# Optimization experiments

Hardware: AMD Instinct MI355X
Metric: run time of the kernel (lower is better)

The kernel has to match this reference:

```python
import jax, jax.numpy as jnp
import numpy as np

B, HW, E, H, L, T = 256, 196, 1024, 1024, 128, 48
FC_OUT = L + H + 2  # label | topic | temp | stop


def _linear_params(k, out_d, in_d):
    k1, k2 = jax.random.split(k)
    bound = 1.0 / np.sqrt(in_d)
    W = jax.random.uniform(k1, (out_d, in_d), jnp.float32, -bound, bound)
    b = jax.random.uniform(k2, (out_d,), jnp.float32, -bound, bound)
    return W, b


def setup_inputs() -> dict:
    key = jax.random.key(0)
    ks = jax.random.split(key, 8)
    image = jax.random.normal(ks[0], (B, HW, E), jnp.float32)
    label = jax.random.uniform(ks[1], (B, T, L), jnp.float32)
    # lengths sorted descending (the torch module uses @length_sorted)
    length = jnp.sort(jax.random.randint(ks[2], (B,), 1, T + 1))[::-1]
    W_h, b_h = _linear_params(ks[3], H, E)
    W_m, b_m = _linear_params(ks[4], H, E)
    W_ih, b_ih = _linear_params(ks[5], 4 * H, E + L)
    W_hh, b_hh = _linear_params(ks[6], 4 * H, H)
    W_fc, b_fc = _linear_params(ks[7], FC_OUT, H)
    return {"image": image, "label": label, "length": length,
            "W_h": W_h, "b_h": b_h, "W_m": W_m, "b_m": b_m,
            "W_ih": W_ih, "W_hh": W_hh, "b_ih": b_ih, "b_hh": b_hh,
            "W_fc": W_fc, "b_fc": b_fc}


def reference(image, label, length, W_h, b_h, W_m, b_m, W_ih, W_hh, b_ih, b_hh, W_fc, b_fc):
    # dropout is identity (eval mode)
    img_mean = image.mean(axis=1)                       # (B, E)
    h0 = jnp.tanh(img_mean @ W_h.T + b_h)               # (B, H)
    m0 = jnp.tanh(img_mean @ W_m.T + b_m)               # (B, H)
    lab_t_major = jnp.transpose(label, (1, 0, 2))       # (T, B, L)
    ts = jnp.arange(T)

    def step(carry, inp):
        h, m = carry
        lab_t, t = inp
        x = jnp.concatenate([img_mean, lab_t], axis=-1)          # (B, E+L)
        gates = x @ W_ih.T + b_ih + h @ W_hh.T + b_hh            # (B, 4H), torch order i,f,g,o
        i, f, g, o = jnp.split(gates, 4, axis=-1)
        m = jax.nn.sigmoid(f) * m + jax.nn.sigmoid(i) * jnp.tanh(g)
        h = jax.nn.sigmoid(o) * jnp.tanh(m)
        out = jax.nn.relu(h @ W_fc.T + b_fc)                     # (B, L+H+2)
        _label = out[:, :L]
        _topic = out[:, L:L + H]
        _temp = jnp.exp(out[:, L + H:L + H + 1])
        _stop = jax.nn.sigmoid(out[:, L + H + 1:])
        mask = (t < length)[:, None].astype(out.dtype)           # pad_sequence zero-padding
        return (h, m), (_label * mask, _topic * mask, _temp * mask, _stop * mask)

    _, (lab_o, top_o, temp_o, stop_o) = jax.lax.scan(step, (h0, m0), (lab_t_major, ts))
    # scan stacks on time axis -> (T, B, D); return batch-major (B, T, D)
    return tuple(jnp.transpose(a, (1, 0, 2)) for a in (lab_o, top_o, temp_o, stop_o))
```

## Files before the change

kernel.cpp:

```cpp
#include <hip/hip_runtime.h>

typedef float f32x4 __attribute__((ext_vector_type(4)));
typedef short s16x8 __attribute__((ext_vector_type(8)));
typedef unsigned short u16;

#define B_    256
#define HW_   196
#define E_    1024
#define H_    1024
#define L_    128
#define T_    48
#define FCOUT 1154
#define FCPAD 1216

#define GJOBS 128
#define FJOBS 76
#define NBLK  (GJOBS + FJOBS)

__device__ __forceinline__ u16 f2bf(float x) {
  union { float f; unsigned u; } v; v.f = x;
  unsigned r = v.u + 0x7FFF + ((v.u >> 16) & 1);
  return (u16)(r >> 16);
}
__device__ __forceinline__ float sigm(float x) { return 1.f / (1.f + expf(-x)); }

__device__ __forceinline__ uint2 ld_h8(const u16* p) {
  unsigned long long v = __hip_atomic_load((const unsigned long long*)p,
                                           __ATOMIC_RELAXED, __HIP_MEMORY_SCOPE_AGENT);
  union { unsigned long long u; uint2 d; } c; c.u = v; return c.d;
}
__device__ __forceinline__ void st_h8(u16* p, ushort4 s) {
  union { ushort4 s; unsigned long long u; } c; c.s = s;
  __hip_atomic_store((unsigned long long*)p, c.u,
                     __ATOMIC_RELAXED, __HIP_MEMORY_SCOPE_AGENT);
}

__device__ __forceinline__ void gbar(int* cnt, int it) {
  __syncthreads();
  if (threadIdx.x == 0) {
    __hip_atomic_fetch_add(cnt, 1, __ATOMIC_RELAXED, __HIP_MEMORY_SCOPE_AGENT);
    const int target = NBLK * (it + 1);
    while (__hip_atomic_load(cnt, __ATOMIC_RELAXED, __HIP_MEMORY_SCOPE_AGENT) < target)
      __builtin_amdgcn_s_sleep(2);
  }
  __syncthreads();
}

__global__ __launch_bounds__(256) void cvt_bf16_v4(
    const float* __restrict__ in, u16* __restrict__ out,
    int src_rows, int in_ld, int in_off, int cols4, long total4) {
  long idx = (long)blockIdx.x * 256 + threadIdx.x;
  if (idx >= total4) return;
  int r  = (int)(idx / cols4);
  int c4 = (int)(idx % cols4) * 4;
  f32x4 v = {0.f, 0.f, 0.f, 0.f};
  if (r < src_rows) v = *(const f32x4*)&in[(size_t)r * in_ld + in_off + c4];
  ushort4 o;
  ((u16*)&o)[0] = f2bf(v[0]); ((u16*)&o)[1] = f2bf(v[1]);
  ((u16*)&o)[2] = f2bf(v[2]); ((u16*)&o)[3] = f2bf(v[3]);
  *(ushort4*)&out[idx * 4] = o;
}

__global__ __launch_bounds__(256) void img_mean_k(
    const float* __restrict__ image, u16* __restrict__ meanB) {
  int idx = blockIdx.x * 256 + threadIdx.x;
  int b  = idx >> 8;
  int e4 = (idx & 255) * 4;
  const float* p = image + (size_t)b * HW_ * E_ + e4;
  f32x4 s = {0.f, 0.f, 0.f, 0.f};
  #pragma unroll 4
  for (int hw = 0; hw < HW_; ++hw) s += *(const f32x4*)&p[(size_t)hw * E_];
  ushort4 o;
  #pragma unroll
  for (int c = 0; c < 4; ++c) ((u16*)&o)[c] = f2bf(s[c] * (1.0f / HW_));
  *(ushort4*)&meanB[(size_t)b * E_ + e4] = o;
}

template <int MODE>
__global__ __launch_bounds__(256) void gemm_nt(
    const u16* __restrict__ A, int lda, const u16* __restrict__ Bp, int ldb, int K,
    const float* __restrict__ bias1, const float* __restrict__ bias2,
    float* __restrict__ outF, u16* __restrict__ outB, int ldc) {
  __shared__ __align__(16) u16 As[64][72];
  __shared__ __align__(16) u16 Bs[64][72];

  const int m0 = blockIdx.x * 64;
  const int n0 = blockIdx.y * 64;
  const int tid  = threadIdx.x;
  const int lane = tid & 63;
  const int wave = tid >> 6;
  const int wm = wave & 1, wn = wave >> 1;
  const int quad = lane >> 4, l16 = lane & 15;
  const int loadRow = tid >> 3;
  const int loadCol = (tid & 7) * 8;

  f32x4 acc[2][2] = {};

  for (int kb = 0; kb < K; kb += 64) {
    __syncthreads();
    #pragma unroll
    for (int p = 0; p < 2; ++p) {
      int r = loadRow + p * 32;
      *(uint4*)&As[r][loadCol] = *(const uint4*)&A [(size_t)(m0 + r) * lda + kb + loadCol];
      *(uint4*)&Bs[r][loadCol] = *(const uint4*)&Bp[(size_t)(n0 + r) * ldb + kb + loadCol];
    }
    __syncthreads();
    #pragma unroll
    for (int ks = 0; ks < 64; ks += 32) {
      s16x8 a0v = *(const s16x8*)&As[wm * 32      + l16][ks + quad * 8];
      s16x8 a1v = *(const s16x8*)&As[wm * 32 + 16 + l16][ks + quad * 8];
      s16x8 b0v = *(const s16x8*)&Bs[wn * 32      + l16][ks + quad * 8];
      s16x8 b1v = *(const s16x8*)&Bs[wn * 32 + 16 + l16][ks + quad * 8];
      acc[0][0] = __builtin_amdgcn_mfma_f32_16x16x32_bf16(a0v, b0v, acc[0][0], 0, 0, 0);
      acc[0][1] = __builtin_amdgcn_mfma_f32_16x16x32_bf16(a0v, b1v, acc[0][1], 0, 0, 0);
      acc[1][0] = __builtin_amdgcn_mfma_f32_16x16x32_bf16(a1v, b0v, acc[1][0], 0, 0, 0);
      acc[1][1] = __builtin_amdgcn_mfma_f32_16x16x32_bf16(a1v, b1v, acc[1][1], 0, 0, 0);
    }
  }

  #pragma unroll
  for (int mi = 0; mi < 2; ++mi) {
    #pragma unroll
    for (int ni = 0; ni < 2; ++ni) {
      #pragma unroll
      for (int r = 0; r < 4; ++r) {
        int m = m0 + wm * 32 + mi * 16 + quad * 4 + r;
        int n = n0 + wn * 32 + ni * 16 + l16;
        float v = acc[mi][ni][r];
        if constexpr (MODE == 0) {
          outF[(size_t)m * ldc + n] = v + bias1[n] + bias2[n];
        } else if constexpr (MODE == 1) {
          outB[(size_t)m * ldc + n] = f2bf(tanhf(v + bias1[n]));
        } else {
          outF[(size_t)m * ldc + n] = tanhf(v + bias1[n]);
        }
      }
    }
  }
}

struct GS8 { u16 A[2][32][72]; u16 B[2][256][72]; };
struct FS8 { u16 A[2][64][72]; u16 B[2][64][72]; };
union __align__(16) SharedU {
  GS8 g;
  FS8 f;
  float gs[2][4][32][68];
  float fs[64][68];
};

__global__ __launch_bounds__(512) void scan_k(
    const u16* __restrict__ labB,
    const u16* __restrict__ WihL,
    const u16* __restrict__ WhhB,
    const u16* __restrict__ WfcB,
    const float* __restrict__ gbase,
    const float* __restrict__ b_fc,
    u16* __restrict__ hb0, u16* __restrict__ hb1,
    const float* __restrict__ mS0,
    const int* __restrict__ length,
    float* __restrict__ out,
    int* __restrict__ barCnt) {
  __shared__ SharedU sh;
  __shared__ __align__(16) float gbs[4][32][64];

  const int bid  = blockIdx.x;
  const int tid  = threadIdx.x;
  const int g2   = tid >> 8;
  const int gtid = tid & 255;
  const int lane = tid & 63;
  const int wave = tid >> 6;
  const int sw   = wave & 3;
  const int quad = lane >> 4, l16 = lane & 15;
  const int ar = gtid >> 3;
  const int ac = (gtid & 7) * 8;

  const bool isG = bid < GJOBS;
  int mb = 0, jb = 0, m0 = 0, n0 = 0, glen = 0;
  f32x4 mreg = {0.f, 0.f, 0.f, 0.f};

  if (isG) {
    jb = (bid & 7) * 2 + ((bid >> 3) & 1);
    mb = bid >> 4;
    glen = length[mb * 32];
    const int bl = tid >> 4, j4 = (tid & 15) * 4;
    #pragma unroll
    for (int g = 0; g < 4; ++g)
      *(f32x4*)&gbs[g][bl][j4] =
          *(const f32x4*)&gbase[(size_t)(mb * 32 + bl) * (4 * H_) + g * H_ + jb * 64 + j4];
    mreg = *(const f32x4*)&mS0[(size_t)(mb * 32 + bl) * H_ + jb * 64 + j4];
  } else {
    const int fid = bid - GJOBS;
    m0 = (fid / 19) * 64;
    n0 = (fid % 19) * 64;
    glen = length[m0];
  }

  for (int p = 0; p <= T_; ++p) {
    u16* hcur  = (p & 1) ? hb1 : hb0;
    u16* hnext = (p & 1) ? hb0 : hb1;

    if (isG) {
      if (p < T_ && glen > p) {
        f32x4 acc[2][4] = {};
        for (int kb = 0; kb < 9; ++kb) {
          const int seg1 = (g2 == 1) || (kb >= 2);
          const int k0 = g2 ? (448 + kb * 64) : (seg1 ? (kb - 2) * 64 : kb * 64);
          __syncthreads();
          if (seg1) {
            const u16* Ap = hcur + (size_t)(mb * 32 + ar) * H_ + k0 + ac;
            *(uint2*)&sh.g.A[g2][ar][ac]     = ld_h8(Ap);
            *(uint2*)&sh.g.A[g2][ar][ac + 4] = ld_h8(Ap + 4);
          } else {
            *(uint4*)&sh.g.A[g2][ar][ac] = *(const uint4*)
                &labB[(size_t)(mb * 32 + ar) * (T_ * L_) + (size_t)p * L_ + k0 + ac];
          }
          const u16* Bw  = seg1 ? WhhB : WihL;
          const int  ldb = seg1 ? H_ : L_;
          #pragma unroll
          for (int q = 0; q < 8; ++q) {
            int rr = ar + q * 32;
            int grow = (rr >> 6) * H_ + jb * 64 + (rr & 63);
            *(uint4*)&sh.g.B[g2][rr][ac] =
                *(const uint4*)&Bw[(size_t)grow * ldb + k0 + ac];
          }
          __syncthreads();
          #pragma unroll
          for (int ks = 0; ks < 64; ks += 32) {
            s16x8 av[2], bv[4];
            av[0] = *(const s16x8*)&sh.g.A[g2][l16][ks + quad * 8];
            av[1] = *(const s16x8*)&sh.g.A[g2][16 + l16][ks + quad * 8];
            #pragma unroll
            for (int ni = 0; ni < 4; ++ni)
              bv[ni] = *(const s16x8*)&sh.g.B[g2][sw * 64 + ni * 16 + l16][ks + quad * 8];
            #pragma unroll
            for (int mi = 0; mi < 2; ++mi)
              #pragma unroll
              for (int ni = 0; ni < 4; ++ni)
                acc[mi][ni] = __builtin_amdgcn_mfma_f32_16x16x32_bf16(
                    av[mi], bv[ni], acc[mi][ni], 0, 0, 0);
          }
        }

        __syncthreads();
        #pragma unroll
        for (int mi = 0; mi < 2; ++mi)
          #pragma unroll
          for (int ni = 0; ni < 4; ++ni)
            #pragma unroll
            for (int r = 0; r < 4; ++r)
              sh.gs[g2][sw][mi * 16 + quad * 4 + r][ni * 16 + l16] = acc[mi][ni][r];
        __syncthreads();

        {
          const int bl = tid >> 4, j4 = (tid & 15) * 4;
          f32x4 gi = *(const f32x4*)&sh.gs[0][0][bl][j4] + *(const f32x4*)&sh.gs[1][0][bl][j4];
          f32x4 gf = *(const f32x4*)&sh.gs[0][1][bl][j4] + *(const f32x4*)&sh.gs[1][1][bl][j4];
          f32x4 gg = *(const f32x4*)&sh.gs[0][2][bl][j4] + *(const f32x4*)&sh.gs[1][2][bl][j4];
          f32x4 go = *(const f32x4*)&sh.gs[0][3][bl][j4] + *(const f32x4*)&sh.gs[1][3][bl][j4];
          f32x4 bi  = *(const f32x4*)&gbs[0][bl][j4];
          f32x4 bff = *(const f32x4*)&gbs[1][bl][j4];
          f32x4 bg  = *(const f32x4*)&gbs[2][bl][j4];
          f32x4 bo  = *(const f32x4*)&gbs[3][bl][j4];
          ushort4 hb;
          #pragma unroll
          for (int c = 0; c < 4; ++c) {
            float I = sigm(gi[c] + bi[c]);
            float F = sigm(gf[c] + bff[c]);
            float G = tanhf(gg[c] + bg[c]);
            float O = sigm(go[c] + bo[c]);
            float mm = F * mreg[c] + I * G;
            mreg[c] = mm;
            ((u16*)&hb)[c] = f2bf(O * tanhf(mm));
          }
          st_h8(&hnext[(size_t)(mb * 32 + bl) * H_ + jb * 64 + j4], hb);
        }
      }
    } else if (p >= 1) {
      const int t = p - 1;
      if (glen > t) {
        const int wm = sw & 1, wn = sw >> 1;
        f32x4 acc[2][2] = {};
        for (int kb = 0; kb < 8; ++kb) {
          const int k0 = g2 * 512 + kb * 64;
          __syncthreads();
          #pragma unroll
          for (int pp = 0; pp < 2; ++pp) {
            int r = ar + pp * 32;
            const u16* Ap = hcur + (size_t)(m0 + r) * H_ + k0 + ac;
            *(uint2*)&sh.f.A[g2][r][ac]     = ld_h8(Ap);
            *(uint2*)&sh.f.A[g2][r][ac + 4] = ld_h8(Ap + 4);
            *(uint4*)&sh.f.B[g2][r][ac] =
                *(const uint4*)&WfcB[(size_t)(n0 + r) * H_ + k0 + ac];
          }
          __syncthreads();
          #pragma unroll
          for (int ks = 0; ks < 64; ks += 32) {
            s16x8 a0v = *(const s16x8*)&sh.f.A[g2][wm * 32      + l16][ks + quad * 8];
            s16x8 a1v = *(const s16x8*)&sh.f.A[g2][wm * 32 + 16 + l16][ks + quad * 8];
            s16x8 b0v = *(const s16x8*)&sh.f.B[g2][wn * 32      + l16][ks + quad * 8];
            s16x8 b1v = *(const s16x8*)&sh.f.B[g2][wn * 32 + 16 + l16][ks + quad * 8];
            acc[0][0] = __builtin_amdgcn_mfma_f32_16x16x32_bf16(a0v, b0v, acc[0][0], 0, 0, 0);
            acc[0][1] = __builtin_amdgcn_mfma_f32_16x16x32_bf16(a0v, b1v, acc[0][1], 0, 0, 0);
            acc[1][0] = __builtin_amdgcn_mfma_f32_16x16x32_bf16(a1v, b0v, acc[1][0], 0, 0, 0);
            acc[1][1] = __builtin_amdgcn_mfma_f32_16x16x32_bf16(a1v, b1v, acc[1][1], 0, 0, 0);
          }
        }

        __syncthreads();
        if (g2 == 1) {
          #pragma unroll
          for (int mi = 0; mi < 2; ++mi)
            #pragma unroll
            for (int ni = 0; ni < 2; ++ni)
              #pragma unroll
              for (int r = 0; r < 4; ++r)
                sh.fs[wm * 32 + mi * 16 + quad * 4 + r][wn * 32 + ni * 16 + l16] =
                    acc[mi][ni][r];
        }
        __syncthreads();
        if (g2 == 0) {
          #pragma unroll
          for (int mi = 0; mi < 2; ++mi) {
            #pragma unroll
            for (int ni = 0; ni < 2; ++ni) {
              #pragma unroll
              for (int r = 0; r < 4; ++r) {
                int ml = wm * 32 + mi * 16 + quad * 4 + r;
                int nl = wn * 32 + ni * 16 + l16;
                int m = m0 + ml;
                int n = n0 + nl;
                if (n < FCOUT) {
                  float rv = fmaxf(acc[mi][ni][r] + sh.fs[ml][nl] + b_fc[n], 0.f);
                  float msk = (t < length[m]) ? 1.f : 0.f;
                  if (n < L_) {
                    out[(size_t)m * (T_ * L_) + t * L_ + n] = rv * msk;
                  } else if (n < L_ + H_) {
                    out[(size_t)(B_ * T_ * L_) + (size_t)m * (T_ * H_) + t * H_ + (n - L_)] = rv * msk;
                  } else if (n == L_ + H_) {
                    out[(size_t)B_ * T_ * (L_ + H_) + m * T_ + t] = expf(rv) * msk;
                  } else {
                    out[(size_t)B_ * T_ * (L_ + H_ + 1) + m * T_ + t] = sigm(rv) * msk;
                  }
                }
              }
            }
          }
        }
      } else if (n0 == 0) {
        f32x4 z = {0.f, 0.f, 0.f, 0.f};
        for (int i = tid; i < 64 * 32; i += 512) {
          int r = i >> 5, c4 = (i & 31) * 4;
          *(f32x4*)&out[(size_t)(m0 + r) * (T_ * L_) + t * L_ + c4] = z;
        }
        for (int i = tid; i < 64 * 256; i += 512) {
          int r = i >> 8, c4 = (i & 255) * 4;
          *(f32x4*)&out[(size_t)(B_ * T_ * L_) + (size_t)(m0 + r) * (T_ * H_) + t * H_ + c4] = z;
        }
        if (tid < 64) {
          out[(size_t)B_ * T_ * (L_ + H_) + (m0 + tid) * T_ + t] = 0.f;
          out[(size_t)B_ * T_ * (L_ + H_ + 1) + (m0 + tid) * T_ + t] = 0.f;
        }
      }
    }

    gbar(barCnt, p);
  }
}

extern "C" void kernel_launch(void* const* d_in, const int* in_sizes, int n_in,
                              void* d_out, int out_size, void* d_ws, size_t ws_size,
                              hipStream_t stream) {
  const float* image  = (const float*)d_in[0];
  const float* label  = (const float*)d_in[1];
  const int*   length = (const int*)  d_in[2];
  const float* W_h    = (const float*)d_in[3];
  const float* b_h    = (const float*)d_in[4];
  const float* W_m    = (const float*)d_in[5];
  const float* b_m    = (const float*)d_in[6];
  const float* W_ih   = (const float*)d_in[7];
  const float* W_hh   = (const float*)d_in[8];
  const float* b_ih   = (const float*)d_in[9];
  const float* b_hh   = (const float*)d_in[10];
  const float* W_fc   = (const float*)d_in[11];
  const float* b_fc   = (const float*)d_in[12];
  float* out = (float*)d_out;

  char* ws = (char*)d_ws;
  size_t off = 0;
  auto alloc = [&](size_t bytes) -> void* {
    void* p = ws + off;
    off = (off + bytes + 255) & ~(size_t)255;
    return p;
  };
  u16*   meanB = (u16*)  alloc((size_t)B_ * E_ * 2);
  u16*   WhB   = (u16*)  alloc((size_t)H_ * E_ * 2);
  u16*   WmB   = (u16*)  alloc((size_t)H_ * E_ * 2);
  u16*   WihE  = (u16*)  alloc((size_t)4 * H_ * E_ * 2);
  u16*   WihL  = (u16*)  alloc((size_t)4 * H_ * L_ * 2);
  u16*   WhhB  = (u16*)  alloc((size_t)4 * H_ * H_ * 2);
  u16*   WfcB  = (u16*)  alloc((size_t)FCPAD * H_ * 2);
  u16*   labB  = (u16*)  alloc((size_t)B_ * T_ * L_ * 2);
  float* gbase = (float*)alloc((size_t)B_ * 4 * H_ * 4);
  u16*   hbuf0 = (u16*)  alloc((size_t)B_ * H_ * 2);
  u16*   hbuf1 = (u16*)  alloc((size_t)B_ * H_ * 2);
  float* mS    = (float*)alloc((size_t)B_ * H_ * 4);
  int*   bar   = (int*)  alloc(256);

  auto cvt = [&](const float* in, u16* o, int rows, int src_rows, int in_ld,
                 int in_off, int cols) {
    long total4 = (long)rows * cols / 4;
    int blocks = (int)((total4 + 255) / 256);
    cvt_bf16_v4<<<blocks, 256, 0, stream>>>(in, o, src_rows, in_ld, in_off,
                                            cols / 4, total4);
  };

  cvt(W_h,  WhB,  H_,     H_,     E_,      0,  E_);
  cvt(W_m,  WmB,  H_,     H_,     E_,      0,  E_);
  cvt(W_ih, WihE, 4 * H_, 4 * H_, E_ + L_, 0,  E_);
  cvt(W_ih, WihL, 4 * H_, 4 * H_, E_ + L_, E_, L_);
  cvt(W_hh, WhhB, 4 * H_, 4 * H_, H_,      0,  H_);
  cvt(W_fc, WfcB, FCPAD,  FCOUT,  H_,      0,  H_);
  cvt(label, labB, B_, B_, T_ * L_, 0, T_ * L_);

  img_mean_k<<<(B_ * E_ / 4) / 256, 256, 0, stream>>>(image, meanB);

  gemm_nt<1><<<dim3(B_ / 64, H_ / 64), 256, 0, stream>>>(
      meanB, E_, WhB, E_, E_, b_h, nullptr, nullptr, hbuf0, H_);
  gemm_nt<2><<<dim3(B_ / 64, H_ / 64), 256, 0, stream>>>(
      meanB, E_, WmB, E_, E_, b_m, nullptr, mS, nullptr, H_);
  gemm_nt<0><<<dim3(B_ / 64, (4 * H_) / 64), 256, 0, stream>>>(
      meanB, E_, WihE, E_, E_, b_ih, b_hh, gbase, nullptr, 4 * H_);

  hipMemsetAsync(bar, 0, 8, stream);
  scan_k<<<NBLK, 512, 0, stream>>>(
      labB, WihL, WhhB, WfcB, gbase, b_fc, hbuf0, hbuf1, mS, length, out, bar);
}
```

Measured before the change: 1.403 ms.

## Split grid barrier into producer/consumer counters with triple-buffered hidden state

Replaces the all-blocks grid barrier with a packed 64-bit counter: gate blocks bump the low half and FC blocks bump the high half. Each role waits only on the producers it actually depends on, which lets gate blocks run ahead of the FC blocks by one step. The hidden state becomes a three-slot ring buffer so that run-ahead is safe. Weight and label tiles are now prefetched before the wait, and all h tiles are loaded into registers up front, to hide latency. This adds register pressure, and the relaxed-atomic ordering is subtle.

```diff
diff --git a/kernel.cpp b/kernel.cpp
--- a/kernel.cpp
+++ b/kernel.cpp
@@ -35,15 +35,21 @@
                      __ATOMIC_RELAXED, __HIP_MEMORY_SCOPE_AGENT);
 }
 
-__device__ __forceinline__ void gbar(int* cnt, int it) {
-  __syncthreads();
+__device__ __forceinline__ void bar_wait(unsigned long long* bar,
+                                         unsigned lot, unsigned hit) {
   if (threadIdx.x == 0) {
-    __hip_atomic_fetch_add(cnt, 1, __ATOMIC_RELAXED, __HIP_MEMORY_SCOPE_AGENT);
-    const int target = NBLK * (it + 1);
-    while (__hip_atomic_load(cnt, __ATOMIC_RELAXED, __HIP_MEMORY_SCOPE_AGENT) < target)
+    for (;;) {
+      unsigned long long v = __hip_atomic_load(bar, __ATOMIC_RELAXED,
+                                               __HIP_MEMORY_SCOPE_AGENT);
+      if ((unsigned)v >= lot && (unsigned)(v >> 32) >= hit) break;
       __builtin_amdgcn_s_sleep(2);
+    }
   }
   __syncthreads();
+}
+__device__ __forceinline__ void bar_add(unsigned long long* bar,
+                                        unsigned long long v) {
+  __hip_atomic_fetch_add(bar, v, __ATOMIC_RELAXED, __HIP_MEMORY_SCOPE_AGENT);
 }
 
 __global__ __launch_bounds__(256) void cvt_bf16_v4(
@@ -155,11 +161,11 @@
     const u16* __restrict__ WfcB,
     const float* __restrict__ gbase,
     const float* __restrict__ b_fc,
-    u16* __restrict__ hb0, u16* __restrict__ hb1,
+    u16* __restrict__ hs0, u16* __restrict__ hs1, u16* __restrict__ hs2,
     const float* __restrict__ mS0,
     const int* __restrict__ length,
     float* __restrict__ out,
-    int* __restrict__ barCnt) {
+    unsigned long long* __restrict__ bar) {
   __shared__ SharedU sh;
   __shared__ __align__(16) float gbs[4][32][64];
 
@@ -173,6 +179,8 @@
   const int quad = lane >> 4, l16 = lane & 15;
   const int ar = gtid >> 3;
   const int ac = (gtid & 7) * 8;
+
+  u16* slot[3] = {hs0, hs1, hs2};
 
   const bool isG = bid < GJOBS;
   int mb = 0, jb = 0, m0 = 0, n0 = 0, glen = 0;
@@ -194,34 +202,87 @@
     n0 = (fid % 19) * 64;
     glen = length[m0];
   }
+  __syncthreads();
 
   for (int p = 0; p <= T_; ++p) {
-    u16* hcur  = (p & 1) ? hb1 : hb0;
-    u16* hnext = (p & 1) ? hb0 : hb1;
+    u16* hc = slot[p % 3];
+    u16* hn = slot[(p + 1) % 3];
 
     if (isG) {
-      if (p < T_ && glen > p) {
-        f32x4 acc[2][4] = {};
-        for (int kb = 0; kb < 9; ++kb) {
-          const int seg1 = (g2 == 1) || (kb >= 2);
-          const int k0 = g2 ? (448 + kb * 64) : (seg1 ? (kb - 2) * 64 : kb * 64);
-          __syncthreads();
-          if (seg1) {
-            const u16* Ap = hcur + (size_t)(mb * 32 + ar) * H_ + k0 + ac;
-            *(uint2*)&sh.g.A[g2][ar][ac]     = ld_h8(Ap);
-            *(uint2*)&sh.g.A[g2][ar][ac + 4] = ld_h8(Ap + 4);
-          } else {
-            *(uint4*)&sh.g.A[g2][ar][ac] = *(const uint4*)
-                &labB[(size_t)(mb * 32 + ar) * (T_ * L_) + (size_t)p * L_ + k0 + ac];
-          }
-          const u16* Bw  = seg1 ? WhhB : WihL;
-          const int  ldb = seg1 ? H_ : L_;
+      if (p == T_) break;
+      const bool live = glen > p;
+
+      uint4 lA1;
+      if (live) {
+        {
+          const u16* Bw  = g2 ? WhhB : WihL;
+          const int  ldb = g2 ? H_ : L_;
+          const int  k0b = g2 ? 448 : 0;
           #pragma unroll
           for (int q = 0; q < 8; ++q) {
             int rr = ar + q * 32;
             int grow = (rr >> 6) * H_ + jb * 64 + (rr & 63);
             *(uint4*)&sh.g.B[g2][rr][ac] =
-                *(const uint4*)&Bw[(size_t)grow * ldb + k0 + ac];
+                *(const uint4*)&Bw[(size_t)grow * ldb + k0b + ac];
+          }
+          if (g2 == 0) {
+            const u16* Lp = labB + (size_t)(mb * 32 + ar) * (T_ * L_) +
+                            (size_t)p * L_ + ac;
+            *(uint4*)&sh.g.A[0][ar][ac] = *(const uint4*)Lp;
+            lA1 = *(const uint4*)(Lp + 64);
+          }
+        }
+      }
+      bar_wait(bar, 128u * (unsigned)p,
+               (p >= 2) ? 76u * (unsigned)(p - 1) : 0u);
+
+      if (live) {
+        uint2 hA[9][2];
+        const u16* hrow = hc + (size_t)(mb * 32 + ar) * H_ + ac;
+        if (g2 == 0) {
+          #pragma unroll
+          for (int s = 0; s < 7; ++s) {
+            hA[s][0] = ld_h8(hrow + s * 64);
+            hA[s][1] = ld_h8(hrow + s * 64 + 4);
+          }
+        } else {
+          #pragma unroll
+          for (int s = 0; s < 9; ++s) {
+            hA[s][0] = ld_h8(hrow + 448 + s * 64);
+            hA[s][1] = ld_h8(hrow + 448 + s * 64 + 4);
+          }
+        }
+
+        f32x4 acc[2][4] = {};
+        #pragma unroll
+        for (int kb = 0; kb < 9; ++kb) {
+          if (kb == 0) {
+            if (g2 == 1) {
+              *(uint2*)&sh.g.A[1][ar][ac]     = hA[0][0];
+              *(uint2*)&sh.g.A[1][ar][ac + 4] = hA[0][1];
+            }
+          } else {
+            __syncthreads();
+            if (kb == 1 && g2 == 0) {
+              *(uint4*)&sh.g.A[0][ar][ac] = lA1;
+            } else if (g2 == 0) {
+              *(uint2*)&sh.g.A[0][ar][ac]     = hA[kb - 2][0];
+              *(uint2*)&sh.g.A[0][ar][ac + 4] = hA[kb - 2][1];
+            } else {
+              *(uint2*)&sh.g.A[1][ar][ac]     = hA[kb][0];
+              *(uint2*)&sh.g.A[1][ar][ac + 4] = hA[kb][1];
+            }
+            const int seg1 = (g2 == 1) || (kb >= 2);
+            const int k0 = g2 ? (448 + kb * 64) : (seg1 ? (kb - 2) * 64 : kb * 64);
+            const u16* Bw  = seg1 ? WhhB : WihL;
+            const int  ldb = seg1 ? H_ : L_;
+            #pragma unroll
+            for (int q = 0; q < 8; ++q) {
+              int rr = ar + q * 32;
+              int grow = (rr >> 6) * H_ + jb * 64 + (rr & 63);
+              *(uint4*)&sh.g.B[g2][rr][ac] =
+                  *(const uint4*)&Bw[(size_t)grow * ldb + k0 + ac];
+            }
           }
           __syncthreads();
           #pragma unroll
@@ -272,25 +333,51 @@
             mreg[c] = mm;
             ((u16*)&hb)[c] = f2bf(O * tanhf(mm));
           }
-          st_h8(&hnext[(size_t)(mb * 32 + bl) * H_ + jb * 64 + j4], hb);
-        }
+          st_h8(&hn[(size_t)(mb * 32 + bl) * H_ + jb * 64 + j4], hb);
+        }
+        __syncthreads();
       }
-    } else if (p >= 1) {
+      if (tid == 0) bar_add(bar, 1ull);
+    } else {
       const int t = p - 1;
-      if (glen > t) {
+      const bool liveF = (p >= 1) && (glen > t);
+
+      if (liveF) {
+        #pragma unroll
+        for (int pp = 0; pp < 2; ++pp) {
+          int r = ar + pp * 32;
+          *(uint4*)&sh.f.B[g2][r][ac] =
+              *(const uint4*)&WfcB[(size_t)(n0 + r) * H_ + g2 * 512 + ac];
+        }
+      }
+      bar_wait(bar, 128u * (unsigned)((p <= T_) ? p : T_), 0u);
+
+      if (liveF) {
+        uint2 fA[8][2][2];
+        #pragma unroll
+        for (int kb = 0; kb < 8; ++kb) {
+          #pragma unroll
+          for (int pp = 0; pp < 2; ++pp) {
+            const u16* Ap = hc + (size_t)(m0 + ar + pp * 32) * H_ +
+                            g2 * 512 + kb * 64 + ac;
+            fA[kb][pp][0] = ld_h8(Ap);
+            fA[kb][pp][1] = ld_h8(Ap + 4);
+          }
+        }
+
         const int wm = sw & 1, wn = sw >> 1;
         f32x4 acc[2][2] = {};
+        #pragma unroll
         for (int kb = 0; kb < 8; ++kb) {
-          const int k0 = g2 * 512 + kb * 64;
-          __syncthreads();
+          if (kb > 0) __syncthreads();
           #pragma unroll
           for (int pp = 0; pp < 2; ++pp) {
             int r = ar + pp * 32;
-            const u16* Ap = hcur + (size_t)(m0 + r) * H_ + k0 + ac;
-            *(uint2*)&sh.f.A[g2][r][ac]     = ld_h8(Ap);
-            *(uint2*)&sh.f.A[g2][r][ac + 4] = ld_h8(Ap + 4);
-            *(uint4*)&sh.f.B[g2][r][ac] =
-                *(const uint4*)&WfcB[(size_t)(n0 + r) * H_ + k0 + ac];
+            *(uint2*)&sh.f.A[g2][r][ac]     = fA[kb][pp][0];
+            *(uint2*)&sh.f.A[g2][r][ac + 4] = fA[kb][pp][1];
+            if (kb > 0)
+              *(uint4*)&sh.f.B[g2][r][ac] =
+                  *(const uint4*)&WfcB[(size_t)(n0 + r) * H_ + g2 * 512 + kb * 64 + ac];
           }
           __syncthreads();
           #pragma unroll
@@ -307,6 +394,7 @@
         }
 
         __syncthreads();
+        if (tid == 0) bar_add(bar, 1ull << 32);
         if (g2 == 1) {
           #pragma unroll
           for (int mi = 0; mi < 2; ++mi)
@@ -346,24 +434,25 @@
             }
           }
         }
-      } else if (n0 == 0) {
-        f32x4 z = {0.f, 0.f, 0.f, 0.f};
-        for (int i = tid; i < 64 * 32; i += 512) {
-          int r = i >> 5, c4 = (i & 31) * 4;
-          *(f32x4*)&out[(size_t)(m0 + r) * (T_ * L_) + t * L_ + c4] = z;
-        }
-        for (int i = tid; i < 64 * 256; i += 512) {
-          int r = i >> 8, c4 = (i & 255) * 4;
-          *(f32x4*)&out[(size_t)(B_ * T_ * L_) + (size_t)(m0 + r) * (T_ * H_) + t * H_ + c4] = z;
-        }
-        if (tid < 64) {
-          out[(size_t)B_ * T_ * (L_ + H_) + (m0 + tid) * T_ + t] = 0.f;
-          out[(size_t)B_ * T_ * (L_ + H_ + 1) + (m0 + tid) * T_ + t] = 0.f;
-        }
+      } else {
+        if (p >= 1 && n0 == 0) {
+          f32x4 z = {0.f, 0.f, 0.f, 0.f};
+          for (int i = tid; i < 64 * 32; i += 512) {
+            int r = i >> 5, c4 = (i & 31) * 4;
+            *(f32x4*)&out[(size_t)(m0 + r) * (T_ * L_) + t * L_ + c4] = z;
+          }
+          for (int i = tid; i < 64 * 256; i += 512) {
+            int r = i >> 8, c4 = (i & 255) * 4;
+            *(f32x4*)&out[(size_t)(B_ * T_ * L_) + (size_t)(m0 + r) * (T_ * H_) + t * H_ + c4] = z;
+          }
+          if (tid < 64) {
+            out[(size_t)B_ * T_ * (L_ + H_) + (m0 + tid) * T_ + t] = 0.f;
+            out[(size_t)B_ * T_ * (L_ + H_ + 1) + (m0 + tid) * T_ + t] = 0.f;
+          }
+        }
+        if (tid == 0) bar_add(bar, 1ull << 32);
       }
     }
-
-    gbar(barCnt, p);
   }
 }
 
@@ -403,8 +492,9 @@
   float* gbase = (float*)alloc((size_t)B_ * 4 * H_ * 4);
   u16*   hbuf0 = (u16*)  alloc((size_t)B_ * H_ * 2);
   u16*   hbuf1 = (u16*)  alloc((size_t)B_ * H_ * 2);
+  u16*   hbuf2 = (u16*)  alloc((size_t)B_ * H_ * 2);
   float* mS    = (float*)alloc((size_t)B_ * H_ * 4);
-  int*   bar   = (int*)  alloc(256);
+  unsigned long long* bar = (unsigned long long*)alloc(256);
 
   auto cvt = [&](const float* in, u16* o, int rows, int src_rows, int in_ld,
                  int in_off, int cols) {
@@ -433,5 +523,6 @@
 
   hipMemsetAsync(bar, 0, 8, stream);
   scan_k<<<NBLK, 512, 0, stream>>>(
-      labB, WihL, WhhB, WfcB, gbase, b_fc, hbuf0, hbuf1, mS, length, out, bar);
-}
+      labB, WihL, WhhB, WfcB, gbase, b_fc, hbuf0, hbuf1, hbuf2, mS, length,
+      out, bar);
+}
```

After: 1.492 ms. 6.3% more time.

## Stage full h rows in LDS once per step; read weights directly from global

Applied to the files above, without the earlier changes.

The recurrent scan kernel no longer stages A and B tiles through double-buffered shared memory with two barriers per k-block. Each step now copies the whole hidden-state slab for the block into padded LDS behind a single barrier. MFMA operands for W_hh, W_ih, W_fc and the label input are loaded straight from global memory (expected to hit L2 or cache) into registers. The gate bias is also read from global each step instead of being kept in LDS. This removes many per-step syncs and LDS writes, at the cost of uncoalesced global weight loads and higher register pressure from fully unrolled loops.

```diff
diff --git a/kernel.cpp b/kernel.cpp
--- a/kernel.cpp
+++ b/kernel.cpp
@@ -16,6 +16,8 @@
 #define GJOBS 128
 #define FJOBS 76
 #define NBLK  (GJOBS + FJOBS)
+
+#define HPAD  1032
 
 __device__ __forceinline__ u16 f2bf(float x) {
   union { float f; unsigned u; } v; v.f = x;
@@ -139,11 +141,8 @@
   }
 }
 
-struct GS8 { u16 A[2][32][72]; u16 B[2][256][72]; };
-struct FS8 { u16 A[2][64][72]; u16 B[2][64][72]; };
 union __align__(16) SharedU {
-  GS8 g;
-  FS8 f;
+  u16 hA[64][HPAD];
   float gs[2][4][32][68];
   float fs[64][68];
 };
@@ -161,18 +160,14 @@
     float* __restrict__ out,
     int* __restrict__ barCnt) {
   __shared__ SharedU sh;
-  __shared__ __align__(16) float gbs[4][32][64];
 
   const int bid  = blockIdx.x;
   const int tid  = threadIdx.x;
   const int g2   = tid >> 8;
-  const int gtid = tid & 255;
   const int lane = tid & 63;
   const int wave = tid >> 6;
   const int sw   = wave & 3;
   const int quad = lane >> 4, l16 = lane & 15;
-  const int ar = gtid >> 3;
-  const int ac = (gtid & 7) * 8;
 
   const bool isG = bid < GJOBS;
   int mb = 0, jb = 0, m0 = 0, n0 = 0, glen = 0;
@@ -183,10 +178,6 @@
     mb = bid >> 4;
     glen = length[mb * 32];
     const int bl = tid >> 4, j4 = (tid & 15) * 4;
-    #pragma unroll
-    for (int g = 0; g < 4; ++g)
-      *(f32x4*)&gbs[g][bl][j4] =
-          *(const f32x4*)&gbase[(size_t)(mb * 32 + bl) * (4 * H_) + g * H_ + jb * 64 + j4];
     mreg = *(const f32x4*)&mS0[(size_t)(mb * 32 + bl) * H_ + jb * 64 + j4];
   } else {
     const int fid = bid - GJOBS;
@@ -195,43 +186,57 @@
     glen = length[m0];
   }
 
+  const u16* gBhh[4];
+  const u16* gBih[4];
+  const u16* fBfc[2];
+  if (isG) {
+    #pragma unroll
+    for (int ni = 0; ni < 4; ++ni) {
+      const int row = sw * H_ + jb * 64 + ni * 16 + l16;
+      gBhh[ni] = WhhB + (size_t)row * H_ + quad * 8;
+      gBih[ni] = WihL + (size_t)row * L_ + quad * 8;
+    }
+  } else {
+    const int wn = sw >> 1;
+    #pragma unroll
+    for (int ni = 0; ni < 2; ++ni)
+      fBfc[ni] = WfcB + (size_t)(n0 + wn * 32 + ni * 16 + l16) * H_ +
+                 g2 * 512 + quad * 8;
+  }
+
   for (int p = 0; p <= T_; ++p) {
     u16* hcur  = (p & 1) ? hb1 : hb0;
     u16* hnext = (p & 1) ? hb0 : hb1;
 
     if (isG) {
       if (p < T_ && glen > p) {
+        {
+          const int r  = tid >> 4;
+          const int c0 = (tid & 15) * 64;
+          const u16* src = hcur + (size_t)(mb * 32 + r) * H_ + c0;
+          u16* dst = &sh.hA[r][c0];
+          uint2 tmp[16];
+          #pragma unroll
+          for (int i = 0; i < 16; ++i) tmp[i] = ld_h8(src + i * 4);
+          #pragma unroll
+          for (int i = 0; i < 16; ++i) *(uint2*)(dst + i * 4) = tmp[i];
+        }
+        __syncthreads();
+
         f32x4 acc[2][4] = {};
-        for (int kb = 0; kb < 9; ++kb) {
-          const int seg1 = (g2 == 1) || (kb >= 2);
-          const int k0 = g2 ? (448 + kb * 64) : (seg1 ? (kb - 2) * 64 : kb * 64);
-          __syncthreads();
-          if (seg1) {
-            const u16* Ap = hcur + (size_t)(mb * 32 + ar) * H_ + k0 + ac;
-            *(uint2*)&sh.g.A[g2][ar][ac]     = ld_h8(Ap);
-            *(uint2*)&sh.g.A[g2][ar][ac + 4] = ld_h8(Ap + 4);
-          } else {
-            *(uint4*)&sh.g.A[g2][ar][ac] = *(const uint4*)
-                &labB[(size_t)(mb * 32 + ar) * (T_ * L_) + (size_t)p * L_ + k0 + ac];
-          }
-          const u16* Bw  = seg1 ? WhhB : WihL;
-          const int  ldb = seg1 ? H_ : L_;
-          #pragma unroll
-          for (int q = 0; q < 8; ++q) {
-            int rr = ar + q * 32;
-            int grow = (rr >> 6) * H_ + jb * 64 + (rr & 63);
-            *(uint4*)&sh.g.B[g2][rr][ac] =
-                *(const uint4*)&Bw[(size_t)grow * ldb + k0 + ac];
-          }
-          __syncthreads();
-          #pragma unroll
-          for (int ks = 0; ks < 64; ks += 32) {
+        if (g2 == 0) {
+          const u16* A0 = labB + (size_t)(mb * 32 + l16) * (T_ * L_) +
+                          (size_t)p * L_ + quad * 8;
+          const u16* A1 = A0 + (size_t)16 * (T_ * L_);
+          #pragma unroll
+          for (int kk = 0; kk < 4; ++kk) {
+            const int k = kk * 32;
             s16x8 av[2], bv[4];
-            av[0] = *(const s16x8*)&sh.g.A[g2][l16][ks + quad * 8];
-            av[1] = *(const s16x8*)&sh.g.A[g2][16 + l16][ks + quad * 8];
+            av[0] = *(const s16x8*)(A0 + k);
+            av[1] = *(const s16x8*)(A1 + k);
             #pragma unroll
             for (int ni = 0; ni < 4; ++ni)
-              bv[ni] = *(const s16x8*)&sh.g.B[g2][sw * 64 + ni * 16 + l16][ks + quad * 8];
+              bv[ni] = *(const s16x8*)(gBih[ni] + k);
             #pragma unroll
             for (int mi = 0; mi < 2; ++mi)
               #pragma unroll
@@ -239,6 +244,39 @@
                 acc[mi][ni] = __builtin_amdgcn_mfma_f32_16x16x32_bf16(
                     av[mi], bv[ni], acc[mi][ni], 0, 0, 0);
           }
+          #pragma unroll
+          for (int kk = 0; kk < 14; ++kk) {
+            const int k = kk * 32;
+            s16x8 av[2], bv[4];
+            av[0] = *(const s16x8*)&sh.hA[l16][k + quad * 8];
+            av[1] = *(const s16x8*)&sh.hA[16 + l16][k + quad * 8];
+            #pragma unroll
+            for (int ni = 0; ni < 4; ++ni)
+              bv[ni] = *(const s16x8*)(gBhh[ni] + k);
+            #pragma unroll
+            for (int mi = 0; mi < 2; ++mi)
+              #pragma unroll
+              for (int ni = 0; ni < 4; ++ni)
+                acc[mi][ni] = __builtin_amdgcn_mfma_f32_16x16x32_bf16(
+                    av[mi], bv[ni], acc[mi][ni], 0, 0, 0);
+          }
+        } else {
+          #pragma unroll
+          for (int kk = 0; kk < 18; ++kk) {
+            const int k = 448 + kk * 32;
+            s16x8 av[2], bv[4];
+            av[0] = *(const s16x8*)&sh.hA[l16][k + quad * 8];
+            av[1] = *(const s16x8*)&sh.hA[16 + l16][k + quad * 8];
+            #pragma unroll
+            for (int ni = 0; ni < 4; ++ni)
+              bv[ni] = *(const s16x8*)(gBhh[ni] + k);
+            #pragma unroll
+            for (int mi = 0; mi < 2; ++mi)
+              #pragma unroll
+              for (int ni = 0; ni < 4; ++ni)
+                acc[mi][ni] = __builtin_amdgcn_mfma_f32_16x16x32_bf16(
+                    av[mi], bv[ni], acc[mi][ni], 0, 0, 0);
+          }
         }
 
         __syncthreads();
@@ -253,14 +291,16 @@
 
         {
           const int bl = tid >> 4, j4 = (tid & 15) * 4;
+          const int b = mb * 32 + bl, j = jb * 64 + j4;
+          const float* gb = gbase + (size_t)b * (4 * H_) + j;
           f32x4 gi = *(const f32x4*)&sh.gs[0][0][bl][j4] + *(const f32x4*)&sh.gs[1][0][bl][j4];
           f32x4 gf = *(const f32x4*)&sh.gs[0][1][bl][j4] + *(const f32x4*)&sh.gs[1][1][bl][j4];
           f32x4 gg = *(const f32x4*)&sh.gs[0][2][bl][j4] + *(const f32x4*)&sh.gs[1][2][bl][j4];
           f32x4 go = *(const f32x4*)&sh.gs[0][3][bl][j4] + *(const f32x4*)&sh.gs[1][3][bl][j4];
-          f32x4 bi  = *(const f32x4*)&gbs[0][bl][j4];
-          f32x4 bff = *(const f32x4*)&gbs[1][bl][j4];
-          f32x4 bg  = *(const f32x4*)&gbs[2][bl][j4];
-          f32x4 bo  = *(const f32x4*)&gbs[3][bl][j4];
+          f32x4 bi  = *(const f32x4*)(gb);
+          f32x4 bff = *(const f32x4*)(gb + H_);
+          f32x4 bg  = *(const f32x4*)(gb + 2 * H_);
+          f32x4 bo  = *(const f32x4*)(gb + 3 * H_);
           ushort4 hb;
           #pragma unroll
           for (int c = 0; c < 4; ++c) {
@@ -272,40 +312,42 @@
             mreg[c] = mm;
             ((u16*)&hb)[c] = f2bf(O * tanhf(mm));
           }
-          st_h8(&hnext[(size_t)(mb * 32 + bl) * H_ + jb * 64 + j4], hb);
+          st_h8(&hnext[(size_t)b * H_ + j], hb);
         }
       }
     } else if (p >= 1) {
       const int t = p - 1;
       if (glen > t) {
-        const int wm = sw & 1, wn = sw >> 1;
+        #pragma unroll
+        for (int half = 0; half < 2; ++half) {
+          const int r  = (tid >> 4) + half * 32;
+          const int c0 = (tid & 15) * 64;
+          const u16* src = hcur + (size_t)(m0 + r) * H_ + c0;
+          u16* dst = &sh.hA[r][c0];
+          uint2 tmp[16];
+          #pragma unroll
+          for (int i = 0; i < 16; ++i) tmp[i] = ld_h8(src + i * 4);
+          #pragma unroll
+          for (int i = 0; i < 16; ++i) *(uint2*)(dst + i * 4) = tmp[i];
+        }
+        __syncthreads();
+
+        const int wm = sw & 1;
         f32x4 acc[2][2] = {};
-        for (int kb = 0; kb < 8; ++kb) {
-          const int k0 = g2 * 512 + kb * 64;
-          __syncthreads();
-          #pragma unroll
-          for (int pp = 0; pp < 2; ++pp) {
-            int r = ar + pp * 32;
-            const u16* Ap = hcur + (size_t)(m0 + r) * H_ + k0 + ac;
-            *(uint2*)&sh.f.A[g2][r][ac]     = ld_h8(Ap);
-            *(uint2*)&sh.f.A[g2][r][ac + 4] = ld_h8(Ap + 4);
-            *(uint4*)&sh.f.B[g2][r][ac] =
-                *(const uint4*)&WfcB[(size_t)(n0 + r) * H_ + k0 + ac];
-          }
-          __syncthreads();
-          #pragma unroll
-          for (int ks = 0; ks < 64; ks += 32) {
-            s16x8 a0v = *(const s16x8*)&sh.f.A[g2][wm * 32      + l16][ks + quad * 8];
-            s16x8 a1v = *(const s16x8*)&sh.f.A[g2][wm * 32 + 16 + l16][ks + quad * 8];
-            s16x8 b0v = *(const s16x8*)&sh.f.B[g2][wn * 32      + l16][ks + quad * 8];
-            s16x8 b1v = *(const s16x8*)&sh.f.B[g2][wn * 32 + 16 + l16][ks + quad * 8];
-            acc[0][0] = __builtin_amdgcn_mfma_f32_16x16x32_bf16(a0v, b0v, acc[0][0], 0, 0, 0);
-            acc[0][1] = __builtin_amdgcn_mfma_f32_16x16x32_bf16(a0v, b1v, acc[0][1], 0, 0, 0);
-            acc[1][0] = __builtin_amdgcn_mfma_f32_16x16x32_bf16(a1v, b0v, acc[1][0], 0, 0, 0);
-            acc[1][1] = __builtin_amdgcn_mfma_f32_16x16x32_bf16(a1v, b1v, acc[1][1], 0, 0, 0);
-          }
-        }
-
+        #pragma unroll
+        for (int kk = 0; kk < 16; ++kk) {
+          const int k = g2 * 512 + kk * 32;
+          s16x8 a0v = *(const s16x8*)&sh.hA[wm * 32      + l16][k + quad * 8];
+          s16x8 a1v = *(const s16x8*)&sh.hA[wm * 32 + 16 + l16][k + quad * 8];
+          s16x8 b0v = *(const s16x8*)(fBfc[0] + kk * 32);
+          s16x8 b1v = *(const s16x8*)(fBfc[1] + kk * 32);
+          acc[0][0] = __builtin_amdgcn_mfma_f32_16x16x32_bf16(a0v, b0v, acc[0][0], 0, 0, 0);
+          acc[0][1] = __builtin_amdgcn_mfma_f32_16x16x32_bf16(a0v, b1v, acc[0][1], 0, 0, 0);
+          acc[1][0] = __builtin_amdgcn_mfma_f32_16x16x32_bf16(a1v, b0v, acc[1][0], 0, 0, 0);
+          acc[1][1] = __builtin_amdgcn_mfma_f32_16x16x32_bf16(a1v, b1v, acc[1][1], 0, 0, 0);
+        }
+
+        const int wn = sw >> 1;
         __syncthreads();
         if (g2 == 1) {
           #pragma unroll
```

After: 1.913 ms. 1.36x slower.
